# Kernel tuning notes

Measured on AMD Instinct MI355X. Metric: run time of the kernel, lower is better.

Reference implementation:

```python
import jax, jax.numpy as jnp
import numpy as np

BETA = 0.95      # snn.Leaky(beta=0.95)
THRESHOLD = 1.0  # snntorch default
STEPS = 10


def setup_inputs() -> dict:
    key = jax.random.key(0)
    k1, k2 = jax.random.split(key)
    x = jax.random.normal(k1, (65536, 784), dtype=jnp.float32)
    # fc weight [out=10, in=784], no bias
    W = jax.random.normal(k2, (10, 784), dtype=jnp.float32) * (1.0 / np.sqrt(784.0))
    return {"x": x, "W": W}


def reference(x, W):
    # x: [B, 784] (already flat); fc(x) is the same every step -> compute once.
    cur = x @ W.T  # [B, 10]
    # snntorch Leaky (reset-by-subtraction):
    #   reset_t = spk_{t-1}; mem_t = beta*mem_{t-1} + cur - reset_t*thr; spk_t = (mem_t > thr)
    def step(carry, _):
        mem, spk = carry
        mem = BETA * mem + cur - spk * THRESHOLD
        spk = (mem > THRESHOLD).astype(cur.dtype)
        return (mem, spk), spk

    init = (jnp.zeros_like(cur), jnp.zeros_like(cur))
    _, spk_rec = jax.lax.scan(step, init, None, length=STEPS)  # [STEPS, B, 10]
    return spk_rec.sum(axis=0)  # [B, 10]
```

## Files before the change

kernel.cpp:

```cpp
#include <hip/hip_runtime.h>


constexpr int ROWS  = 65536;
constexpr int COLS  = 784;
constexpr int NOUT  = 10;
constexpr int STEPS = 10;

constexpr int BR   = 64;
constexpr int TW   = 16;
constexpr int NT   = COLS / TW;
constexpr int PADW = 17;
constexpr int NH   = 8;
constexpr int CPH  = TW / NH;
constexpr int TPP  = 4;
constexpr int NP   = 12;
constexpr int NBUF = 8;

constexpr int BUF_F = BR * PADW;

__global__ void w_prep(const float* __restrict__ W, double* __restrict__ W64T) {
    int i = blockIdx.x * 256 + threadIdx.x;
    if (i < NOUT * COLS) {
        int c = i / NOUT, j = i - c * NOUT;
        W64T[i] = (double)W[(size_t)j * COLS + c];
    }
}

__global__ __launch_bounds__(512, 8)
void snn_fused(const float* __restrict__ x, const double* __restrict__ W64T,
               float* __restrict__ out) {
    __shared__ __align__(16) char smem[NBUF * BUF_F * 4];
    float*  bufs = reinterpret_cast<float*>(smem);
    double* comb = reinterpret_cast<double*>(smem);

    const int tid = threadIdx.x;
    const int r   = tid & 63;
    const int hu  = __builtin_amdgcn_readfirstlane(tid >> 6);
    const size_t row0 = (size_t)blockIdx.x * BR;
    const float* xblk = x + row0 * COLS;

    auto issueP = [&](int P, float4* v) {
        #pragma unroll
        for (int k = 0; k < 2; ++k) {
            int s = tid + 512 * k;
            int row = s >> 4, seg = s & 15;
            int t  = P * TPP + (seg >> 2);
            int tc = (t < NT) ? t : NT - 1;
            v[k] = *reinterpret_cast<const float4*>(
                xblk + (size_t)row * COLS + tc * TW + (seg & 3) * 4);
        }
    };
    auto wldsP = [&](int P, const float4* v) {
        #pragma unroll
        for (int k = 0; k < 2; ++k) {
            int s = tid + 512 * k;
            int row = s >> 4, seg = s & 15;
            int t  = P * TPP + (seg >> 2);
            int tc = (t < NT) ? t : NT - 1;
            float* p = bufs + (tc & (NBUF - 1)) * BUF_F + row * PADW + (seg & 3) * 4;
            p[0] = v[k].x; p[1] = v[k].y; p[2] = v[k].z; p[3] = v[k].w;
        }
    };

    double acc[NOUT];
    #pragma unroll
    for (int j = 0; j < NOUT; ++j) acc[j] = 0.0;

    float4 v0[2], v1[2];
    issueP(0, v0); wldsP(0, v0);
    issueP(1, v1);
    __syncthreads();

    for (int p = 0; p < NP; ++p) {
        wldsP(p + 1, v1);
        if (p + 2 <= NP) issueP(p + 2, v0);

        #pragma unroll 1
        for (int u = 0; u < TPP; ++u) {
            const int tt = p * TPP + u;
            const float*  src = bufs + (tt & (NBUF - 1)) * BUF_F + r * PADW + hu * CPH;
            const double* wb  = W64T + (size_t)(tt * TW + hu * CPH) * NOUT;
            #pragma unroll
            for (int c = 0; c < CPH; ++c) {
                double xd = (double)src[c];
                #pragma unroll
                for (int j = 0; j < NOUT; ++j)
                    acc[j] = fma(xd, wb[c * NOUT + j], acc[j]);
            }
        }
        __syncthreads();
        v1[0] = v0[0]; v1[1] = v0[1];
    }

    {
        const int tt = NT - 1;
        const float*  src = bufs + (tt & (NBUF - 1)) * BUF_F + r * PADW + hu * CPH;
        const double* wb  = W64T + (size_t)(tt * TW + hu * CPH) * NOUT;
        #pragma unroll
        for (int c = 0; c < CPH; ++c) {
            double xd = (double)src[c];
            #pragma unroll
            for (int j = 0; j < NOUT; ++j)
                acc[j] = fma(xd, wb[c * NOUT + j], acc[j]);
        }
    }

    #pragma unroll 1
    for (int half = 0; half < 2; ++half) {
        __syncthreads();
        if ((r >> 5) == half) {
            #pragma unroll
            for (int j = 0; j < NOUT; ++j)
                comb[(hu * 32 + (r & 31)) * NOUT + j] = acc[j];
        }
        __syncthreads();
        for (int i = tid; i < 32 * NOUT; i += 512) {
            double c0 = comb[i]                  + comb[32 * NOUT + i];
            double c1 = comb[2 * 32 * NOUT + i]  + comb[3 * 32 * NOUT + i];
            double c2 = comb[4 * 32 * NOUT + i]  + comb[5 * 32 * NOUT + i];
            double c3 = comb[6 * 32 * NOUT + i]  + comb[7 * 32 * NOUT + i];
            double cur = (c0 + c1) + (c2 + c3);

            double mem = 0.0, spk = 0.0, s = 0.0;
            #pragma unroll
            for (int st = 0; st < STEPS; ++st) {
                mem = 0.95 * mem + cur - spk;
                spk = (mem > 1.0) ? 1.0 : 0.0;
                s  += spk;
            }
            out[(row0 + half * 32) * NOUT + i] = (float)s;
        }
    }
}

extern "C" void kernel_launch(void* const* d_in, const int* in_sizes, int n_in,
                              void* d_out, int out_size, void* d_ws, size_t ws_size,
                              hipStream_t stream) {
    const float* x = (const float*)d_in[0];
    const float* W = (const float*)d_in[1];
    float*  out  = (float*)d_out;
    double* W64T = (double*)d_ws;

    hipLaunchKernelGGL(w_prep, dim3((NOUT * COLS + 255) / 256), dim3(256), 0, stream, W, W64T);
    hipLaunchKernelGGL(snn_fused, dim3(ROWS / BR), dim3(512), 0, stream, x, W64T, out);
}
```

Before: 49.63 us.

## Compute matmul in fp32 with error-bounded fp64 recompute near spike threshold

Switches the main x·Wᵀ accumulation from fp64 to fp32 FMAs and tracks the row norm of x alongside it. A Cauchy-Schwarz error bound (||x||·||W_j|| times a constant) flags rows whose membrane trajectory comes close to the threshold, and only those are recomputed exactly in fp64 from global memory. This removes the heavy fp64 FMA cost of the inner loop. In exchange it adds a norm-reduction prep kernel, a divergent fallback path per output, and relies on a hand-chosen error constant for correctness.

Result: slower. 156.7 us (+215.8%).

```diff
diff --git a/kernel.cpp b/kernel.cpp
--- a/kernel.cpp
+++ b/kernel.cpp
@@ -15,23 +15,38 @@
 constexpr int TPP  = 4;
 constexpr int NP   = 12;
 constexpr int NBUF = 8;
-
 constexpr int BUF_F = BR * PADW;
 
-__global__ void w_prep(const float* __restrict__ W, double* __restrict__ W64T) {
-    int i = blockIdx.x * 256 + threadIdx.x;
-    if (i < NOUT * COLS) {
-        int c = i / NOUT, j = i - c * NOUT;
-        W64T[i] = (double)W[(size_t)j * COLS + c];
+constexpr int WT_BYTES = NOUT * COLS * 4;
+
+__global__ __launch_bounds__(256)
+void w_prep(const float* __restrict__ W, float* __restrict__ W32T,
+            double* __restrict__ wn) {
+    __shared__ double red[256];
+    const int j = blockIdx.x;
+    const int t = threadIdx.x;
+    double nrm = 0.0;
+    for (int c = t; c < COLS; c += 256) {
+        float w = W[(size_t)j * COLS + c];
+        W32T[(size_t)c * NOUT + j] = w;
+        nrm = fma((double)w, (double)w, nrm);
     }
+    red[t] = nrm;
+    __syncthreads();
+    for (int s = 128; s > 0; s >>= 1) {
+        if (t < s) red[t] += red[t + s];
+        __syncthreads();
+    }
+    if (t == 0) wn[j] = sqrt(red[0]);
 }
 
 __global__ __launch_bounds__(512, 8)
-void snn_fused(const float* __restrict__ x, const double* __restrict__ W64T,
+void snn_fused(const float* __restrict__ x, const float* __restrict__ W,
+               const float* __restrict__ W32T, const double* __restrict__ wn,
                float* __restrict__ out) {
     __shared__ __align__(16) char smem[NBUF * BUF_F * 4];
-    float*  bufs = reinterpret_cast<float*>(smem);
-    double* comb = reinterpret_cast<double*>(smem);
+    float* bufs = reinterpret_cast<float*>(smem);
+    float* comb = reinterpret_cast<float*>(smem);
 
     const int tid = threadIdx.x;
     const int r   = tid & 63;
@@ -62,9 +77,10 @@
         }
     };
 
-    double acc[NOUT];
+    float sacc[NOUT];
     #pragma unroll
-    for (int j = 0; j < NOUT; ++j) acc[j] = 0.0;
+    for (int j = 0; j < NOUT; ++j) sacc[j] = 0.0f;
+    float nacc = 0.0f;
 
     float4 v0[2], v1[2];
     issueP(0, v0); wldsP(0, v0);
@@ -78,14 +94,15 @@
         #pragma unroll 1
         for (int u = 0; u < TPP; ++u) {
             const int tt = p * TPP + u;
-            const float*  src = bufs + (tt & (NBUF - 1)) * BUF_F + r * PADW + hu * CPH;
-            const double* wb  = W64T + (size_t)(tt * TW + hu * CPH) * NOUT;
+            const float* src = bufs + (tt & (NBUF - 1)) * BUF_F + r * PADW + hu * CPH;
+            const float* wb  = W32T + (size_t)(tt * TW + hu * CPH) * NOUT;
             #pragma unroll
             for (int c = 0; c < CPH; ++c) {
-                double xd = (double)src[c];
+                float xv = src[c];
+                nacc = fmaf(xv, xv, nacc);
                 #pragma unroll
                 for (int j = 0; j < NOUT; ++j)
-                    acc[j] = fma(xd, wb[c * NOUT + j], acc[j]);
+                    sacc[j] = fmaf(xv, wb[c * NOUT + j], sacc[j]);
             }
         }
         __syncthreads();
@@ -94,42 +111,67 @@
 
     {
         const int tt = NT - 1;
-        const float*  src = bufs + (tt & (NBUF - 1)) * BUF_F + r * PADW + hu * CPH;
-        const double* wb  = W64T + (size_t)(tt * TW + hu * CPH) * NOUT;
+        const float* src = bufs + (tt & (NBUF - 1)) * BUF_F + r * PADW + hu * CPH;
+        const float* wb  = W32T + (size_t)(tt * TW + hu * CPH) * NOUT;
         #pragma unroll
         for (int c = 0; c < CPH; ++c) {
-            double xd = (double)src[c];
+            float xv = src[c];
+            nacc = fmaf(xv, xv, nacc);
             #pragma unroll
             for (int j = 0; j < NOUT; ++j)
-                acc[j] = fma(xd, wb[c * NOUT + j], acc[j]);
+                sacc[j] = fmaf(xv, wb[c * NOUT + j], sacc[j]);
         }
     }
+    __syncthreads();
 
-    #pragma unroll 1
-    for (int half = 0; half < 2; ++half) {
-        __syncthreads();
-        if ((r >> 5) == half) {
-            #pragma unroll
-            for (int j = 0; j < NOUT; ++j)
-                comb[(hu * 32 + (r & 31)) * NOUT + j] = acc[j];
+    #pragma unroll
+    for (int j = 0; j < NOUT; ++j)
+        comb[(hu * BR + r) * 11 + j] = sacc[j];
+    comb[(hu * BR + r) * 11 + 10] = nacc;
+    __syncthreads();
+
+    for (int i = tid; i < BR * NOUT; i += 512) {
+        const int rr = i / NOUT, j = i - rr * NOUT;
+        double cur = 0.0, nr2 = 0.0;
+        #pragma unroll
+        for (int o = 0; o < NH; ++o) {
+            cur += (double)comb[(o * BR + rr) * 11 + j];
+            nr2 += (double)comb[(o * BR + rr) * 11 + 10];
         }
-        __syncthreads();
-        for (int i = tid; i < 32 * NOUT; i += 512) {
-            double c0 = comb[i]                  + comb[32 * NOUT + i];
-            double c1 = comb[2 * 32 * NOUT + i]  + comb[3 * 32 * NOUT + i];
-            double c2 = comb[4 * 32 * NOUT + i]  + comb[5 * 32 * NOUT + i];
-            double c3 = comb[6 * 32 * NOUT + i]  + comb[7 * 32 * NOUT + i];
-            double cur = (c0 + c1) + (c2 + c3);
+        const double Emem = 9.7e-5 * sqrt(nr2) * wn[j];
 
-            double mem = 0.0, spk = 0.0, s = 0.0;
+        double mem = 0.0, spk = 0.0, s = 0.0, minm = 1e300;
+        #pragma unroll
+        for (int st = 0; st < STEPS; ++st) {
+            mem = 0.95 * mem + cur - spk;
+            double d = mem - 1.0;
+            minm = fmin(minm, fabs(d));
+            spk = (d > 0.0) ? 1.0 : 0.0;
+            s  += spk;
+        }
+
+        if (minm <= Emem) {
+            const float* xr = x + (row0 + rr) * COLS;
+            const float* wr = W + (size_t)j * COLS;
+            double a0 = 0.0, a1 = 0.0, a2 = 0.0, a3 = 0.0;
+            for (int c = 0; c < COLS; c += 4) {
+                float4 xv = *reinterpret_cast<const float4*>(xr + c);
+                float4 wv = *reinterpret_cast<const float4*>(wr + c);
+                a0 = fma((double)xv.x, (double)wv.x, a0);
+                a1 = fma((double)xv.y, (double)wv.y, a1);
+                a2 = fma((double)xv.z, (double)wv.z, a2);
+                a3 = fma((double)xv.w, (double)wv.w, a3);
+            }
+            double ce = (a0 + a1) + (a2 + a3);
+            mem = 0.0; spk = 0.0; s = 0.0;
             #pragma unroll
             for (int st = 0; st < STEPS; ++st) {
-                mem = 0.95 * mem + cur - spk;
+                mem = 0.95 * mem + ce - spk;
                 spk = (mem > 1.0) ? 1.0 : 0.0;
                 s  += spk;
             }
-            out[(row0 + half * 32) * NOUT + i] = (float)s;
         }
+        out[row0 * NOUT + i] = (float)s;
     }
 }
 
@@ -139,8 +181,10 @@
     const float* x = (const float*)d_in[0];
     const float* W = (const float*)d_in[1];
     float*  out  = (float*)d_out;
-    double* W64T = (double*)d_ws;
+    float*  W32T = (float*)d_ws;
+    double* wnrm = (double*)((char*)d_ws + WT_BYTES);
 
-    hipLaunchKernelGGL(w_prep, dim3((NOUT * COLS + 255) / 256), dim3(256), 0, stream, W, W64T);
-    hipLaunchKernelGGL(snn_fused, dim3(ROWS / BR), dim3(512), 0, stream, x, W64T, out);
+    hipLaunchKernelGGL(w_prep, dim3(NOUT), dim3(256), 0, stream, W, W32T, wnrm);
+    hipLaunchKernelGGL(snn_fused, dim3(ROWS / BR), dim3(512), 0, stream,
+                       x, W, W32T, wnrm, out);
 }
```
